# Optimization experiments

Hardware: AMD Instinct MI355X
Metric: run time of the kernel (lower is better)

## Reference

```python
import jax, jax.numpy as jnp
import numpy as np

T, N, E = 8, 5000, 160000
IN_DIM, HID, H = 64, 128, 8
D = HID // H  # head dim = 16
NC = 2
EPS = 1e-5


def layer_norm(x, g, b):
    mu = jnp.mean(x, axis=-1, keepdims=True)
    var = jnp.mean((x - mu) ** 2, axis=-1, keepdims=True)
    return (x - mu) / jnp.sqrt(var + EPS) * g + b


def setup_inputs() -> dict:
    key = jax.random.key(0)
    ks = jax.random.split(key, 24)
    p = {}
    p["x"] = jax.random.normal(ks[0], (T, N, IN_DIM), dtype=jnp.float32)
    p["edge_index"] = jax.random.randint(ks[1], (T, 2, E), 0, N, dtype=jnp.int32)
    p["noise"] = jax.random.normal(ks[2], (N, HID), dtype=jnp.float32)
    def w(k, shape, fan_in):
        return jax.random.normal(k, shape, dtype=jnp.float32) * (1.0 / np.sqrt(fan_in))
    p["W_proj"] = w(ks[3], (IN_DIM, HID), IN_DIM)
    p["b_proj"] = jnp.zeros((HID,), jnp.float32)
    p["W_gat"] = w(ks[4], (HID, HID), HID)
    p["a_src"] = w(ks[5], (H, D), D)
    p["a_dst"] = w(ks[6], (H, D), D)
    p["b_gat"] = jnp.zeros((HID,), jnp.float32)
    p["g1"] = jnp.ones((HID,), jnp.float32)
    p["be1"] = jnp.zeros((HID,), jnp.float32)
    p["W_qkv"] = w(ks[7], (3 * HID, HID), HID)
    p["b_qkv"] = jnp.zeros((3 * HID,), jnp.float32)
    p["W_o"] = w(ks[8], (HID, HID), HID)
    p["b_o"] = jnp.zeros((HID,), jnp.float32)
    p["g2"] = jnp.ones((HID,), jnp.float32)
    p["be2"] = jnp.zeros((HID,), jnp.float32)
    p["Wc1"] = w(ks[9], (HID, HID), HID)
    p["bc1"] = jnp.zeros((HID,), jnp.float32)
    p["gc"] = jnp.ones((HID,), jnp.float32)
    p["bec"] = jnp.zeros((HID,), jnp.float32)
    p["Wc2"] = w(ks[10], (HID, NC), HID)
    p["bc2"] = jnp.array([0.0, 0.1], jnp.float32)
    return p


def reference(x, edge_index, noise, W_proj, b_proj, W_gat, a_src, a_dst, b_gat,
              g1, be1, W_qkv, b_qkv, W_o, b_o, g2, be2,
              Wc1, bc1, gc, bec, Wc2, bc2):
    # per-timestep projection + ReLU: [T, N, HID]
    h = jax.nn.relu(x @ W_proj + b_proj)

    loop = jnp.arange(N, dtype=edge_index.dtype)

    def gat(h_t, ei):  # h_t: [N, HID], ei: [2, E]
        src = jnp.concatenate([ei[0], loop])  # add self loops
        dst = jnp.concatenate([ei[1], loop])
        xh = (h_t @ W_gat).reshape(N, H, D)          # [N, H, D]
        a_s = jnp.sum(xh * a_src, axis=-1)           # [N, H]
        a_d = jnp.sum(xh * a_dst, axis=-1)           # [N, H]
        e = jax.nn.leaky_relu(a_s[src] + a_d[dst], 0.2)  # [E', H]
        m = jax.ops.segment_max(e, dst, num_segments=N)
        ex = jnp.exp(e - m[dst])
        s = jax.ops.segment_sum(ex, dst, num_segments=N)
        alpha = ex / (s[dst] + 1e-16)                # segment softmax per dst/head
        out = jax.ops.segment_sum(xh[src] * alpha[..., None], dst, num_segments=N)
        return out.reshape(N, HID) + b_gat

    feats = jax.vmap(gat)(h, edge_index)             # [T, N, HID]
    nf = jnp.transpose(feats, (1, 0, 2))             # [N, T, HID] (node = batch)

    nrm = layer_norm(nf, g1, be1)
    qkv = nrm @ W_qkv.T + b_qkv                      # [N, T, 3*HID]
    q, k, v = jnp.split(qkv, 3, axis=-1)
    def heads(t):
        return t.reshape(N, T, H, D).transpose(0, 2, 1, 3)  # [N, H, T, D]
    q, k, v = heads(q), heads(k), heads(v)
    scores = jnp.einsum('nhqd,nhkd->nhqk', q, k) / jnp.sqrt(jnp.float32(D))
    attn = jax.nn.softmax(scores, axis=-1)
    ta = jnp.einsum('nhqk,nhkd->nhqd', attn, v)
    ta = ta.transpose(0, 2, 1, 3).reshape(N, T, HID) @ W_o.T + b_o

    fused = layer_norm(nf + ta, g2, be2)
    emb = fused[:, -1, :]                            # [N, HID]

    node_ids = jnp.arange(N, dtype=jnp.float32) / N
    div = jnp.sin(node_ids * 6.28) * 0.1             # [N]
    emb = emb + div[:, None] + noise * 0.05          # eval noise scale

    h1 = emb @ Wc1 + bc1
    h1 = jax.nn.gelu(layer_norm(h1, gc, bec), approximate=False)
    logits = h1 @ Wc2 + bc2                          # [N, 2]
    sinu = jnp.sin(jnp.arange(N, dtype=jnp.float32) * 0.5) * 0.2
    logits = logits.at[:, 1].add(sinu)
    return emb, logits
```

## Files before the change

kernel.cpp:

```cpp
#include <hip/hip_runtime.h>
#include <math.h>

#define T 8
#define N 5000
#define E 160000
#define EN (E + N)
#define IN_DIM 64
#define HID 128
#define H 8
#define D 16
#define NC 2
#define MT 32

__device__ __forceinline__ float leaky(float e) { return (e >= 0.0f) ? e : 0.2f * e; }

__global__ __launch_bounds__(256) void k_pg(const float* __restrict__ x,
                                            const float* __restrict__ Wp,
                                            const float* __restrict__ bp,
                                            const float* __restrict__ Wg,
                                            const float* __restrict__ asrc,
                                            const float* __restrict__ adst,
                                            float* __restrict__ xh,
                                            float* __restrict__ a_s,
                                            float* __restrict__ a_d,
                                            int* __restrict__ cursor) {
    __shared__ float xt[MT][IN_DIM];
    __shared__ float ht[MT][HID + 1];
    int row0 = blockIdx.x * MT;
    int tid = threadIdx.x;

    {
        int gi = blockIdx.x * 256 + tid;
        if (gi < T * N) cursor[gi] = 0;
    }

    for (int idx = tid; idx < MT * IN_DIM; idx += 256) {
        int r = idx >> 6, k = idx & 63;
        xt[r][k] = x[(size_t)(row0 + r) * IN_DIM + k];
    }
    __syncthreads();

    int cg = tid & 31;
    int rg = tid >> 5;
    int c0 = cg * 4, r0 = rg * 4;

    {
        float4 b4 = *(const float4*)(bp + c0);
        float a00=b4.x,a01=b4.y,a02=b4.z,a03=b4.w;
        float a10=b4.x,a11=b4.y,a12=b4.z,a13=b4.w;
        float a20=b4.x,a21=b4.y,a22=b4.z,a23=b4.w;
        float a30=b4.x,a31=b4.y,a32=b4.z,a33=b4.w;
        for (int k = 0; k < IN_DIM; ++k) {
            float4 w = *(const float4*)(Wp + (size_t)k * HID + c0);
            float x0 = xt[r0 + 0][k], x1 = xt[r0 + 1][k];
            float x2 = xt[r0 + 2][k], x3 = xt[r0 + 3][k];
            a00 += x0*w.x; a01 += x0*w.y; a02 += x0*w.z; a03 += x0*w.w;
            a10 += x1*w.x; a11 += x1*w.y; a12 += x1*w.z; a13 += x1*w.w;
            a20 += x2*w.x; a21 += x2*w.y; a22 += x2*w.z; a23 += x2*w.w;
            a30 += x3*w.x; a31 += x3*w.y; a32 += x3*w.z; a33 += x3*w.w;
        }
        ht[r0+0][c0+0]=fmaxf(a00,0.f); ht[r0+0][c0+1]=fmaxf(a01,0.f);
        ht[r0+0][c0+2]=fmaxf(a02,0.f); ht[r0+0][c0+3]=fmaxf(a03,0.f);
        ht[r0+1][c0+0]=fmaxf(a10,0.f); ht[r0+1][c0+1]=fmaxf(a11,0.f);
        ht[r0+1][c0+2]=fmaxf(a12,0.f); ht[r0+1][c0+3]=fmaxf(a13,0.f);
        ht[r0+2][c0+0]=fmaxf(a20,0.f); ht[r0+2][c0+1]=fmaxf(a21,0.f);
        ht[r0+2][c0+2]=fmaxf(a22,0.f); ht[r0+2][c0+3]=fmaxf(a23,0.f);
        ht[r0+3][c0+0]=fmaxf(a30,0.f); ht[r0+3][c0+1]=fmaxf(a31,0.f);
        ht[r0+3][c0+2]=fmaxf(a32,0.f); ht[r0+3][c0+3]=fmaxf(a33,0.f);
    }
    __syncthreads();

    float a00=0,a01=0,a02=0,a03=0, a10=0,a11=0,a12=0,a13=0;
    float a20=0,a21=0,a22=0,a23=0, a30=0,a31=0,a32=0,a33=0;
    for (int k = 0; k < HID; ++k) {
        float4 w = *(const float4*)(Wg + (size_t)k * HID + c0);
        float h0 = ht[r0 + 0][k], h1 = ht[r0 + 1][k];
        float h2 = ht[r0 + 2][k], h3 = ht[r0 + 3][k];
        a00 += h0*w.x; a01 += h0*w.y; a02 += h0*w.z; a03 += h0*w.w;
        a10 += h1*w.x; a11 += h1*w.y; a12 += h1*w.z; a13 += h1*w.w;
        a20 += h2*w.x; a21 += h2*w.y; a22 += h2*w.z; a23 += h2*w.w;
        a30 += h3*w.x; a31 += h3*w.y; a32 += h3*w.z; a33 += h3*w.w;
    }
    {
        float4 v;
        v.x=a00; v.y=a01; v.z=a02; v.w=a03;
        *(float4*)(xh + (size_t)(row0 + r0 + 0) * HID + c0) = v;
        v.x=a10; v.y=a11; v.z=a12; v.w=a13;
        *(float4*)(xh + (size_t)(row0 + r0 + 1) * HID + c0) = v;
        v.x=a20; v.y=a21; v.z=a22; v.w=a23;
        *(float4*)(xh + (size_t)(row0 + r0 + 2) * HID + c0) = v;
        v.x=a30; v.y=a31; v.z=a32; v.w=a33;
        *(float4*)(xh + (size_t)(row0 + r0 + 3) * HID + c0) = v;
    }
    __syncthreads();
    ht[r0+0][c0+0]=a00; ht[r0+0][c0+1]=a01; ht[r0+0][c0+2]=a02; ht[r0+0][c0+3]=a03;
    ht[r0+1][c0+0]=a10; ht[r0+1][c0+1]=a11; ht[r0+1][c0+2]=a12; ht[r0+1][c0+3]=a13;
    ht[r0+2][c0+0]=a20; ht[r0+2][c0+1]=a21; ht[r0+2][c0+2]=a22; ht[r0+2][c0+3]=a23;
    ht[r0+3][c0+0]=a30; ht[r0+3][c0+1]=a31; ht[r0+3][c0+2]=a32; ht[r0+3][c0+3]=a33;
    __syncthreads();

    {
        int r = tid >> 3, hh = tid & 7;
        float s1 = 0.0f, s2 = 0.0f;
        #pragma unroll
        for (int d = 0; d < D; ++d) {
            float v = ht[r][hh * D + d];
            s1 += v * asrc[hh * D + d];
            s2 += v * adst[hh * D + d];
        }
        a_s[(size_t)(row0 + r) * H + hh] = s1;
        a_d[(size_t)(row0 + r) * H + hh] = s2;
    }
}

__global__ void k_tr(const float* __restrict__ W_qkv, const float* __restrict__ W_o,
                     float* __restrict__ WTq, float* __restrict__ WoT) {
    int idx = blockIdx.x * 256 + threadIdx.x;
    if (idx < 384 * 128) {
        int j = idx >> 7, c = idx & 127;
        WTq[c * 384 + j] = W_qkv[idx];
    } else if (idx < 384 * 128 + 128 * 128) {
        int r = idx - 384 * 128;
        int j = r >> 7, k = r & 127;
        WoT[k * 128 + j] = W_o[r];
    }
}

__global__ __launch_bounds__(256) void k_hist(const int* __restrict__ ei,
                                              int* __restrict__ cursor) {
    __shared__ int hist[N];
    int t = blockIdx.x >> 3;
    int chunk = blockIdx.x & 7;
    int tid = threadIdx.x;

    for (int i = tid; i < N; i += 256) hist[i] = 0;
    __syncthreads();

    const int CS = (EN + 7) / 8;
    int i0 = chunk * CS;
    int i1 = (i0 + CS < EN) ? i0 + CS : EN;
    const int* drow = ei + (size_t)(2 * t + 1) * E;
    for (int i = i0 + tid; i < i1; i += 256) {
        int d = (i < E) ? drow[i] : (i - E);
        atomicAdd(&hist[d], 1);
    }
    __syncthreads();

    int* cur = cursor + t * N;
    for (int i = tid; i < N; i += 256) {
        int c = hist[i];
        if (c) atomicAdd(&cur[i], c);
    }
}

__global__ void k_scan(int* __restrict__ cursor, int* __restrict__ offs) {
    __shared__ int part[256];
    int t = blockIdx.x;
    int tid = threadIdx.x;
    const int CH = 20;
    int begin = tid * CH;
    int sum = 0;
    for (int k = 0; k < CH; ++k) {
        int i = begin + k;
        if (i < N) sum += cursor[t * N + i];
    }
    part[tid] = sum;
    __syncthreads();
    if (tid == 0) {
        int run = 0;
        for (int i = 0; i < 256; ++i) { int v = part[i]; part[i] = run; run += v; }
        offs[t * (N + 1) + N] = run;
    }
    __syncthreads();
    int run = part[tid];
    for (int k = 0; k < CH; ++k) {
        int i = begin + k;
        if (i < N) {
            int cnt = cursor[t * N + i];
            offs[t * (N + 1) + i] = run;
            cursor[t * N + i] = run;
            run += cnt;
        }
    }
}

__global__ __launch_bounds__(256) void k_scatter(const int* __restrict__ ei,
                                                 int* __restrict__ cursor,
                                                 int* __restrict__ csr_src) {
    const int PT = EN / 4;
    int idx = blockIdx.x * 256 + threadIdx.x;
    int t = idx / PT;
    if (t >= T) return;
    int e0 = idx - t * PT;

    const int* srow = ei + (size_t)(2 * t) * E;
    const int* drow = srow + E;
    int s[4], d[4];
    #pragma unroll
    for (int j = 0; j < 4; ++j) {
        int i = e0 + j * PT;
        if (i < E) { s[j] = srow[i]; d[j] = drow[i]; }
        else       { s[j] = d[j] = i - E; }
    }
    int* cur = cursor + t * N;
    int p[4];
    #pragma unroll
    for (int j = 0; j < 4; ++j) p[j] = atomicAdd(&cur[d[j]], 1);
    int* csb = csr_src + (size_t)t * EN;
    #pragma unroll
    for (int j = 0; j < 4; ++j) csb[p[j]] = s[j];
}

__global__ __launch_bounds__(128) void k_aggc(
        const int* __restrict__ offs, const int* __restrict__ csr_src,
        const float* __restrict__ a_s, const float* __restrict__ a_d,
        const float* __restrict__ xh, const float* __restrict__ b_gat,
        const float* __restrict__ g1, const float* __restrict__ be1,
        float* __restrict__ nrm, float* __restrict__ xlast_g) {
    int b = blockIdx.x;
    int t = b & 7;
    int dst = b >> 3;
    int tid = threadIdx.x;

    int o0 = offs[t * (N + 1) + dst];
    int o1 = offs[t * (N + 1) + dst + 1];
    int deg = o1 - o0;
    const int* esrc = csr_src + (size_t)t * EN + o0;
    const float* as_b = a_s + (size_t)t * N * H;
    const float* ad_b = a_d + (size_t)t * N * H;
    const float* xh_b = xh + (size_t)t * N * HID;

    __shared__ float lal[16][H];
    __shared__ int   lsrc[16];
    __shared__ float ws_s[2][H];
    __shared__ float pacc[2][HID];
    __shared__ float red[128];

    int eh_e = tid >> 3, eh_h = tid & 7;
    int el = tid >> 5, cg = tid & 31;
    int hg = cg >> 2;
    float adh_e = ad_b[dst * H + eh_h];

    float4 acc = {0.0f, 0.0f, 0.0f, 0.0f};
    float wpart = 0.0f;

    int ntile = (deg + 15) >> 4;
    for (int tt = 0; tt < ntile; ++tt) {
        int ej = (tt << 4) + eh_e;
        float w = 0.0f;
        int src = 0;
        if (ej < deg) {
            src = esrc[ej];
            w = expf(leaky(as_b[src * H + eh_h] + adh_e));
        }
        if (eh_h == 0) lsrc[eh_e] = src;
        lal[eh_e][eh_h] = w;
        wpart += w;
        __syncthreads();
        #pragma unroll
        for (int jj = 0; jj < 4; ++jj) {
            int j = (jj << 2) + el;
            int s = lsrc[j];
            float l = lal[j][hg];
            float4 v = *(const float4*)(xh_b + (size_t)s * HID + (cg << 2));
            acc.x += l * v.x; acc.y += l * v.y;
            acc.z += l * v.z; acc.w += l * v.w;
        }
        __syncthreads();
    }

    {
        float w = wpart;
        w += __shfl_xor(w, 8);
        w += __shfl_xor(w, 16);
        w += __shfl_xor(w, 32);
        if ((tid & 63) < 8) ws_s[tid >> 6][eh_h] = w;
    }
    acc.x += __shfl_xor(acc.x, 32);
    acc.y += __shfl_xor(acc.y, 32);
    acc.z += __shfl_xor(acc.z, 32);
    acc.w += __shfl_xor(acc.w, 32);
    if (!(tid & 32)) *(float4*)&pacc[tid >> 6][(tid & 31) << 2] = acc;
    __syncthreads();

    int hh = tid >> 4;
    float wsum = ws_s[0][hh] + ws_s[1][hh];
    float val = (pacc[0][tid] + pacc[1][tid]) / (wsum + 1e-16f);

    float v = val + b_gat[tid];
    red[tid] = v;
    __syncthreads();
    if (tid < 64) {
        float s = red[tid] + red[tid + 64];
        #pragma unroll
        for (int m = 1; m < 64; m <<= 1) s += __shfl_xor(s, m);
        if (tid == 0) red[0] = s;
    }
    __syncthreads();
    float mu = red[0] * (1.0f / HID);
    __syncthreads();
    float dv = v - mu;
    red[tid] = dv * dv;
    __syncthreads();
    if (tid < 64) {
        float s = red[tid] + red[tid + 64];
        #pragma unroll
        for (int m = 1; m < 64; m <<= 1) s += __shfl_xor(s, m);
        if (tid == 0) red[0] = s;
    }
    __syncthreads();
    float rstd = rsqrtf(red[0] * (1.0f / HID) + 1e-5f);

    nrm[(size_t)(t * N + dst) * HID + tid] = dv * rstd * g1[tid] + be1[tid];
    if (t == T - 1) xlast_g[(size_t)dst * HID + tid] = v;
}

__global__ __launch_bounds__(256) void k_qkv(const float* __restrict__ nrm,
                                             const float* __restrict__ WTq,
                                             const float* __restrict__ b_qkv,
                                             float* __restrict__ kv,
                                             float* __restrict__ qlast) {
    __shared__ float at[MT][HID];
    const int NKV = (T * N) / MT;
    int b = blockIdx.x;
    int tid = threadIdx.x;
    bool qp = (b >= NKV);
    int row0 = qp ? (b - NKV) * MT : b * MT;
    const float* src = qp ? nrm + (size_t)(T - 1) * N * HID : nrm;
    int rmax = qp ? N : T * N;

    for (int idx = tid; idx < MT * HID; idx += 256) {
        int r = idx >> 7, c = idx & 127;
        int row = row0 + r;
        at[r][c] = (row < rmax) ? src[(size_t)row * HID + c] : 0.0f;
    }
    __syncthreads();

    int cg = tid & 31, rg = tid >> 5;
    int c0 = cg * 4, r0 = rg * 4;

    int gb = qp ? 0 : 1, ge = qp ? 1 : 3;
    for (int g = gb; g < ge; ++g) {
        int co = g * 128 + c0;
        float4 b4 = *(const float4*)(b_qkv + co);
        float a00=b4.x,a01=b4.y,a02=b4.z,a03=b4.w;
        float a10=b4.x,a11=b4.y,a12=b4.z,a13=b4.w;
        float a20=b4.x,a21=b4.y,a22=b4.z,a23=b4.w;
        float a30=b4.x,a31=b4.y,a32=b4.z,a33=b4.w;
        for (int k = 0; k < HID; ++k) {
            float4 w = *(const float4*)(WTq + (size_t)k * 384 + co);
            float e0 = at[r0 + 0][k], e1 = at[r0 + 1][k];
            float e2 = at[r0 + 2][k], e3 = at[r0 + 3][k];
            a00 += e0*w.x; a01 += e0*w.y; a02 += e0*w.z; a03 += e0*w.w;
            a10 += e1*w.x; a11 += e1*w.y; a12 += e1*w.z; a13 += e1*w.w;
            a20 += e2*w.x; a21 += e2*w.y; a22 += e2*w.z; a23 += e2*w.w;
            a30 += e3*w.x; a31 += e3*w.y; a32 += e3*w.z; a33 += e3*w.w;
        }
        float4 v0; v0.x=a00; v0.y=a01; v0.z=a02; v0.w=a03;
        float4 v1; v1.x=a10; v1.y=a11; v1.z=a12; v1.w=a13;
        float4 v2; v2.x=a20; v2.y=a21; v2.z=a22; v2.w=a23;
        float4 v3; v3.x=a30; v3.y=a31; v3.z=a32; v3.w=a33;
        if (qp) {
            if (row0 + r0 + 0 < N) *(float4*)(qlast + (size_t)(row0+r0+0) * HID + c0) = v0;
            if (row0 + r0 + 1 < N) *(float4*)(qlast + (size_t)(row0+r0+1) * HID + c0) = v1;
            if (row0 + r0 + 2 < N) *(float4*)(qlast + (size_t)(row0+r0+2) * HID + c0) = v2;
            if (row0 + r0 + 3 < N) *(float4*)(qlast + (size_t)(row0+r0+3) * HID + c0) = v3;
        } else {
            int coff = (g - 1) * 128 + c0;
            *(float4*)(kv + (size_t)(row0+r0+0) * 256 + coff) = v0;
            *(float4*)(kv + (size_t)(row0+r0+1) * 256 + coff) = v1;
            *(float4*)(kv + (size_t)(row0+r0+2) * 256 + coff) = v2;
            *(float4*)(kv + (size_t)(row0+r0+3) * 256 + coff) = v3;
        }
    }
}

__global__ __launch_bounds__(128) void k_node(
        const float* __restrict__ kv, const float* __restrict__ qlast,
        const float* __restrict__ xlast_g,
        const float* __restrict__ WoT, const float* __restrict__ b_o,
        const float* __restrict__ g2, const float* __restrict__ be2,
        const float* __restrict__ noise, float* __restrict__ out) {
    __shared__ float ql[HID];
    __shared__ float kl[H][T][D];
    __shared__ float vl[H][T][D];
    __shared__ float attn_l[H][T];
    __shared__ float ta[HID];
    __shared__ float red[128];

    int n = blockIdx.x;
    int tid = threadIdx.x;
    int hh = tid >> 4, dd = tid & 15;

    ql[tid] = qlast[(size_t)n * HID + tid];
    #pragma unroll
    for (int tt = 0; tt < T; ++tt) {
        const float* kvr = kv + (size_t)(tt * N + n) * 256;
        kl[hh][tt][dd] = kvr[tid];
        vl[hh][tt][dd] = kvr[128 + tid];
    }
    float xl = xlast_g[(size_t)n * HID + tid];
    __syncthreads();

    if (tid < H) {
        int hq = tid;
        float sc[T];
        float mx = -1e30f;
        #pragma unroll
        for (int tk = 0; tk < T; ++tk) {
            float a = 0.0f;
            #pragma unroll
            for (int d2 = 0; d2 < D; ++d2) a += ql[hq * D + d2] * kl[hq][tk][d2];
            a *= 0.25f;
            sc[tk] = a;
            mx = fmaxf(mx, a);
        }
        float ssum = 0.0f;
        #pragma unroll
        for (int tk = 0; tk < T; ++tk) { sc[tk] = expf(sc[tk] - mx); ssum += sc[tk]; }
        float inv = 1.0f / ssum;
        #pragma unroll
        for (int tk = 0; tk < T; ++tk) attn_l[hq][tk] = sc[tk] * inv;
    }
    __syncthreads();

    {
        float a = 0.0f;
        #pragma unroll
        for (int tk = 0; tk < T; ++tk) a += attn_l[hh][tk] * vl[hh][tk][dd];
        ta[tid] = a;
    }
    __syncthreads();

    float o = b_o[tid];
    #pragma unroll 8
    for (int k = 0; k < HID; k += 4) {
        float4 t4 = *(const float4*)&ta[k];
        o += t4.x * WoT[(size_t)(k + 0) * 128 + tid]
           + t4.y * WoT[(size_t)(k + 1) * 128 + tid]
           + t4.z * WoT[(size_t)(k + 2) * 128 + tid]
           + t4.w * WoT[(size_t)(k + 3) * 128 + tid];
    }
    float x2 = xl + o;

    red[tid] = x2;
    __syncthreads();
    if (tid < 64) {
        float s = red[tid] + red[tid + 64];
        #pragma unroll
        for (int m = 1; m < 64; m <<= 1) s += __shfl_xor(s, m);
        if (tid == 0) red[0] = s;
    }
    __syncthreads();
    float mu2 = red[0] * (1.0f / HID);
    __syncthreads();
    float d2v = x2 - mu2;
    red[tid] = d2v * d2v;
    __syncthreads();
    if (tid < 64) {
        float s = red[tid] + red[tid + 64];
        #pragma unroll
        for (int m = 1; m < 64; m <<= 1) s += __shfl_xor(s, m);
        if (tid == 0) red[0] = s;
    }
    __syncthreads();
    float rstd2 = rsqrtf(red[0] * (1.0f / HID) + 1e-5f);

    float div = sinf(((float)n / (float)N) * 6.28f) * 0.1f;
    float emb = d2v * rstd2 * g2[tid] + be2[tid]
              + div + noise[(size_t)n * HID + tid] * 0.05f;
    out[(size_t)n * HID + tid] = emb;
}

__global__ __launch_bounds__(256) void k_cls(const float* __restrict__ emb,
                                             const float* __restrict__ Wc1,
                                             const float* __restrict__ bc1,
                                             const float* __restrict__ gc,
                                             const float* __restrict__ bec,
                                             const float* __restrict__ Wc2,
                                             const float* __restrict__ bc2,
                                             float* __restrict__ out) {
    __shared__ float et[MT][HID];
    __shared__ float h1t[MT][HID + 1];
    int row0 = blockIdx.x * MT;
    int tid = threadIdx.x;

    for (int idx = tid; idx < MT * HID; idx += 256) {
        int r = idx >> 7, c = idx & 127;
        int row = row0 + r;
        et[r][c] = (row < N) ? emb[(size_t)row * HID + c] : 0.0f;
    }
    __syncthreads();

    {
        int cg = tid & 31, rg = tid >> 5;
        int c0 = cg * 4, r0 = rg * 4;
        float4 b4 = *(const float4*)(bc1 + c0);
        float a00=b4.x,a01=b4.y,a02=b4.z,a03=b4.w;
        float a10=b4.x,a11=b4.y,a12=b4.z,a13=b4.w;
        float a20=b4.x,a21=b4.y,a22=b4.z,a23=b4.w;
        float a30=b4.x,a31=b4.y,a32=b4.z,a33=b4.w;
        for (int k = 0; k < HID; ++k) {
            float4 w = *(const float4*)(Wc1 + (size_t)k * HID + c0);
            float e0 = et[r0 + 0][k], e1 = et[r0 + 1][k];
            float e2 = et[r0 + 2][k], e3 = et[r0 + 3][k];
            a00 += e0*w.x; a01 += e0*w.y; a02 += e0*w.z; a03 += e0*w.w;
            a10 += e1*w.x; a11 += e1*w.y; a12 += e1*w.z; a13 += e1*w.w;
            a20 += e2*w.x; a21 += e2*w.y; a22 += e2*w.z; a23 += e2*w.w;
            a30 += e3*w.x; a31 += e3*w.y; a32 += e3*w.z; a33 += e3*w.w;
        }
        h1t[r0+0][c0+0]=a00; h1t[r0+0][c0+1]=a01; h1t[r0+0][c0+2]=a02; h1t[r0+0][c0+3]=a03;
        h1t[r0+1][c0+0]=a10; h1t[r0+1][c0+1]=a11; h1t[r0+1][c0+2]=a12; h1t[r0+1][c0+3]=a13;
        h1t[r0+2][c0+0]=a20; h1t[r0+2][c0+1]=a21; h1t[r0+2][c0+2]=a22; h1t[r0+2][c0+3]=a23;
        h1t[r0+3][c0+0]=a30; h1t[r0+3][c0+1]=a31; h1t[r0+3][c0+2]=a32; h1t[r0+3][c0+3]=a33;
    }
    __syncthreads();

    {
        int r = tid >> 3, l = tid & 7;
        float p = 0.0f;
        #pragma unroll
        for (int k = 0; k < 16; ++k) p += h1t[r][l + 8 * k];
        #pragma unroll
        for (int m = 1; m < 8; m <<= 1) p += __shfl_xor(p, m);
        float mu = p * (1.0f / HID);
        float v = 0.0f;
        #pragma unroll
        for (int k = 0; k < 16; ++k) { float d = h1t[r][l + 8 * k] - mu; v += d * d; }
        #pragma unroll
        for (int m = 1; m < 8; m <<= 1) v += __shfl_xor(v, m);
        float rstd = rsqrtf(v * (1.0f / HID) + 1e-5f);
        #pragma unroll
        for (int k = 0; k < 16; ++k) {
            int c = l + 8 * k;
            float lnv = (h1t[r][c] - mu) * rstd * gc[c] + bec[c];
            h1t[r][c] = 0.5f * lnv * (1.0f + erff(lnv * 0.70710678118f));
        }
    }
    __syncthreads();

    if (tid < MT * NC) {
        int r = tid >> 1, j = tid & 1;
        int row = row0 + r;
        if (row < N) {
            float acc = bc2[j];
            #pragma unroll 8
            for (int c = 0; c < HID; ++c) acc += h1t[r][c] * Wc2[c * NC + j];
            if (j == 1) acc += sinf((float)row * 0.5f) * 0.2f;
            out[(size_t)N * HID + (size_t)row * NC + j] = acc;
        }
    }
}

extern "C" void kernel_launch(void* const* d_in, const int* in_sizes, int n_in,
                              void* d_out, int out_size, void* d_ws, size_t ws_size,
                              hipStream_t stream) {
    const float* x      = (const float*)d_in[0];
    const int*   ei     = (const int*)d_in[1];
    const float* noise  = (const float*)d_in[2];
    const float* W_proj = (const float*)d_in[3];
    const float* b_proj = (const float*)d_in[4];
    const float* W_gat  = (const float*)d_in[5];
    const float* a_src  = (const float*)d_in[6];
    const float* a_dst  = (const float*)d_in[7];
    const float* b_gat  = (const float*)d_in[8];
    const float* g1     = (const float*)d_in[9];
    const float* be1    = (const float*)d_in[10];
    const float* W_qkv  = (const float*)d_in[11];
    const float* b_qkv  = (const float*)d_in[12];
    const float* W_o    = (const float*)d_in[13];
    const float* b_o    = (const float*)d_in[14];
    const float* g2     = (const float*)d_in[15];
    const float* be2    = (const float*)d_in[16];
    const float* Wc1    = (const float*)d_in[17];
    const float* bc1    = (const float*)d_in[18];
    const float* gc     = (const float*)d_in[19];
    const float* bec    = (const float*)d_in[20];
    const float* Wc2    = (const float*)d_in[21];
    const float* bc2    = (const float*)d_in[22];
    float* out = (float*)d_out;

    float* xh     = (float*)d_ws;
    float* nrm    = xh + 5120000;
    float* a_s    = nrm + 5120000;
    float* a_d    = a_s + 320000;
    int*   offs    = (int*)(a_d + 320000);
    int*   cursor  = offs + 40008;
    int*   csr_src = cursor + 40000;
    float* WTq    = (float*)(csr_src + 1320000);
    float* WoT    = WTq + 49152;
    float* kv     = WoT + 16384;
    float* qlast  = kv + 10240000;
    float* xlastg = qlast + 640000;

    k_tr<<<(384 * 128 + 128 * 128 + 255) / 256, 256, 0, stream>>>(W_qkv, W_o, WTq, WoT);

    k_pg<<<T * N / MT, 256, 0, stream>>>(x, W_proj, b_proj, W_gat, a_src, a_dst,
                                         xh, a_s, a_d, cursor);

    k_hist<<<T * 8, 256, 0, stream>>>(ei, cursor);
    k_scan<<<T, 256, 0, stream>>>(cursor, offs);
    k_scatter<<<(T * (EN / 4) + 255) / 256, 256, 0, stream>>>(ei, cursor, csr_src);

    k_aggc<<<T * N, 128, 0, stream>>>(offs, csr_src, a_s, a_d, xh,
                                      b_gat, g1, be1, nrm, xlastg);

    k_qkv<<<(T * N) / MT + (N + MT - 1) / MT, 256, 0, stream>>>(nrm, WTq, b_qkv,
                                                                kv, qlast);

    k_node<<<N, 128, 0, stream>>>(kv, qlast, xlastg, WoT, b_o,
                                  g2, be2, noise, out);

    k_cls<<<(N + MT - 1) / MT, 256, 0, stream>>>(out, Wc1, bc1, gc, bec, Wc2, bc2, out);
}
```

Measured before the change: 393.4 us.

## Fuse QKV projection and temporal attention into one per-node-group kernel

Changes the nrm layout to node-major [N,T,HID] so each block can load all timesteps for 4 nodes, then computes K/V for those rows and Q for the last step in shared memory. Attention, output projection, residual and LayerNorm follow in the same kernel. This removes the large global kv/qlast intermediate buffers and one kernel launch. In exchange, k_aggc now writes with a strided pattern, and the LayerNorm switches to a single-pass E[x^2]-mu^2 variance.

```diff
diff --git a/kernel.cpp b/kernel.cpp
--- a/kernel.cpp
+++ b/kernel.cpp
@@ -11,6 +11,7 @@
 #define D 16
 #define NC 2
 #define MT 32
+#define NB 4
 
 __device__ __forceinline__ float leaky(float e) { return (e >= 0.0f) ? e : 0.2f * e; }
 
@@ -311,37 +312,43 @@
     __syncthreads();
     float rstd = rsqrtf(red[0] * (1.0f / HID) + 1e-5f);
 
-    nrm[(size_t)(t * N + dst) * HID + tid] = dv * rstd * g1[tid] + be1[tid];
+    nrm[(size_t)(dst * T + t) * HID + tid] = dv * rstd * g1[tid] + be1[tid];
     if (t == T - 1) xlast_g[(size_t)dst * HID + tid] = v;
 }
 
-__global__ __launch_bounds__(256) void k_qkv(const float* __restrict__ nrm,
-                                             const float* __restrict__ WTq,
-                                             const float* __restrict__ b_qkv,
-                                             float* __restrict__ kv,
-                                             float* __restrict__ qlast) {
-    __shared__ float at[MT][HID];
-    const int NKV = (T * N) / MT;
-    int b = blockIdx.x;
+__global__ __launch_bounds__(256) void k_fuse(
+        const float* __restrict__ nrm,
+        const float* __restrict__ WTq,
+        const float* __restrict__ b_qkv,
+        const float* __restrict__ xlast_g,
+        const float* __restrict__ WoT,
+        const float* __restrict__ b_o,
+        const float* __restrict__ g2, const float* __restrict__ be2,
+        const float* __restrict__ noise, float* __restrict__ out) {
+    __shared__ float at[NB * T][HID];
+    __shared__ float kvl[2][NB * T][HID + 2];
+    __shared__ float ql[NB][HID];
+    float* attn_s = &at[0][0];
+    float* ta_s   = &at[0][0] + 256;
+
+    int n0 = blockIdx.x * NB;
     int tid = threadIdx.x;
-    bool qp = (b >= NKV);
-    int row0 = qp ? (b - NKV) * MT : b * MT;
-    const float* src = qp ? nrm + (size_t)(T - 1) * N * HID : nrm;
-    int rmax = qp ? N : T * N;
-
-    for (int idx = tid; idx < MT * HID; idx += 256) {
-        int r = idx >> 7, c = idx & 127;
-        int row = row0 + r;
-        at[r][c] = (row < rmax) ? src[(size_t)row * HID + c] : 0.0f;
+
+    {
+        const float* src = nrm + (size_t)n0 * T * HID;
+        for (int idx = tid; idx < NB * T * 32; idx += 256) {
+            int r = idx >> 5, c4 = (idx & 31) << 2;
+            *(float4*)&at[r][c4] = *(const float4*)(src + (size_t)r * HID + c4);
+        }
     }
     __syncthreads();
 
     int cg = tid & 31, rg = tid >> 5;
     int c0 = cg * 4, r0 = rg * 4;
 
-    int gb = qp ? 0 : 1, ge = qp ? 1 : 3;
-    for (int g = gb; g < ge; ++g) {
-        int co = g * 128 + c0;
+    #pragma unroll
+    for (int g = 0; g < 2; ++g) {
+        int co = 128 + g * 128 + c0;
         float4 b4 = *(const float4*)(b_qkv + co);
         float a00=b4.x,a01=b4.y,a02=b4.z,a03=b4.w;
         float a10=b4.x,a11=b4.y,a12=b4.z,a13=b4.w;
@@ -349,127 +356,106 @@
         float a30=b4.x,a31=b4.y,a32=b4.z,a33=b4.w;
         for (int k = 0; k < HID; ++k) {
             float4 w = *(const float4*)(WTq + (size_t)k * 384 + co);
-            float e0 = at[r0 + 0][k], e1 = at[r0 + 1][k];
-            float e2 = at[r0 + 2][k], e3 = at[r0 + 3][k];
+            float e0 = at[r0+0][k], e1 = at[r0+1][k];
+            float e2 = at[r0+2][k], e3 = at[r0+3][k];
             a00 += e0*w.x; a01 += e0*w.y; a02 += e0*w.z; a03 += e0*w.w;
             a10 += e1*w.x; a11 += e1*w.y; a12 += e1*w.z; a13 += e1*w.w;
             a20 += e2*w.x; a21 += e2*w.y; a22 += e2*w.z; a23 += e2*w.w;
             a30 += e3*w.x; a31 += e3*w.y; a32 += e3*w.z; a33 += e3*w.w;
         }
-        float4 v0; v0.x=a00; v0.y=a01; v0.z=a02; v0.w=a03;
-        float4 v1; v1.x=a10; v1.y=a11; v1.z=a12; v1.w=a13;
-        float4 v2; v2.x=a20; v2.y=a21; v2.z=a22; v2.w=a23;
-        float4 v3; v3.x=a30; v3.y=a31; v3.z=a32; v3.w=a33;
-        if (qp) {
-            if (row0 + r0 + 0 < N) *(float4*)(qlast + (size_t)(row0+r0+0) * HID + c0) = v0;
-            if (row0 + r0 + 1 < N) *(float4*)(qlast + (size_t)(row0+r0+1) * HID + c0) = v1;
-            if (row0 + r0 + 2 < N) *(float4*)(qlast + (size_t)(row0+r0+2) * HID + c0) = v2;
-            if (row0 + r0 + 3 < N) *(float4*)(qlast + (size_t)(row0+r0+3) * HID + c0) = v3;
-        } else {
-            int coff = (g - 1) * 128 + c0;
-            *(float4*)(kv + (size_t)(row0+r0+0) * 256 + coff) = v0;
-            *(float4*)(kv + (size_t)(row0+r0+1) * 256 + coff) = v1;
-            *(float4*)(kv + (size_t)(row0+r0+2) * 256 + coff) = v2;
-            *(float4*)(kv + (size_t)(row0+r0+3) * 256 + coff) = v3;
-        }
-    }
-}
-
-__global__ __launch_bounds__(128) void k_node(
-        const float* __restrict__ kv, const float* __restrict__ qlast,
-        const float* __restrict__ xlast_g,
-        const float* __restrict__ WoT, const float* __restrict__ b_o,
-        const float* __restrict__ g2, const float* __restrict__ be2,
-        const float* __restrict__ noise, float* __restrict__ out) {
-    __shared__ float ql[HID];
-    __shared__ float kl[H][T][D];
-    __shared__ float vl[H][T][D];
-    __shared__ float attn_l[H][T];
-    __shared__ float ta[HID];
-    __shared__ float red[128];
-
-    int n = blockIdx.x;
-    int tid = threadIdx.x;
-    int hh = tid >> 4, dd = tid & 15;
-
-    ql[tid] = qlast[(size_t)n * HID + tid];
-    #pragma unroll
-    for (int tt = 0; tt < T; ++tt) {
-        const float* kvr = kv + (size_t)(tt * N + n) * 256;
-        kl[hh][tt][dd] = kvr[tid];
-        vl[hh][tt][dd] = kvr[128 + tid];
-    }
-    float xl = xlast_g[(size_t)n * HID + tid];
-    __syncthreads();
-
-    if (tid < H) {
-        int hq = tid;
-        float sc[T];
-        float mx = -1e30f;
+        kvl[g][r0+0][c0+0]=a00; kvl[g][r0+0][c0+1]=a01; kvl[g][r0+0][c0+2]=a02; kvl[g][r0+0][c0+3]=a03;
+        kvl[g][r0+1][c0+0]=a10; kvl[g][r0+1][c0+1]=a11; kvl[g][r0+1][c0+2]=a12; kvl[g][r0+1][c0+3]=a13;
+        kvl[g][r0+2][c0+0]=a20; kvl[g][r0+2][c0+1]=a21; kvl[g][r0+2][c0+2]=a22; kvl[g][r0+2][c0+3]=a23;
+        kvl[g][r0+3][c0+0]=a30; kvl[g][r0+3][c0+1]=a31; kvl[g][r0+3][c0+2]=a32; kvl[g][r0+3][c0+3]=a33;
+    }
+
+    {
+        int u = tid >> 6, c = tid & 63;
+        float q0 = b_qkv[c], q1 = b_qkv[c + 64];
+        const float* ar = at[u * T + (T - 1)];
+        for (int k = 0; k < HID; ++k) {
+            float av = ar[k];
+            q0 += av * WTq[(size_t)k * 384 + c];
+            q1 += av * WTq[(size_t)k * 384 + c + 64];
+        }
+        ql[u][c] = q0;
+        ql[u][c + 64] = q1;
+    }
+    __syncthreads();
+
+    {
+        int u = tid >> 6, h = (tid >> 3) & 7, tk = tid & 7;
+        float qf[D];
+        #pragma unroll
+        for (int d = 0; d < D; ++d) qf[d] = ql[u][h * D + d];
+        const float* kr = &kvl[0][u * T + tk][h * D];
+        float a = 0.0f;
+        #pragma unroll
+        for (int d = 0; d < D; ++d) a += qf[d] * kr[d];
+        a *= 0.25f;
+        float mx = a;
+        mx = fmaxf(mx, __shfl_xor(mx, 1));
+        mx = fmaxf(mx, __shfl_xor(mx, 2));
+        mx = fmaxf(mx, __shfl_xor(mx, 4));
+        float w = expf(a - mx);
+        float ssum = w;
+        ssum += __shfl_xor(ssum, 1);
+        ssum += __shfl_xor(ssum, 2);
+        ssum += __shfl_xor(ssum, 4);
+        attn_s[u * 64 + h * 8 + tk] = w / ssum;
+    }
+    __syncthreads();
+
+    {
+        int u = tid >> 6, c = tid & 63;
+        int ha = c >> 4, hb = (c + 64) >> 4;
+        const float* aa = attn_s + u * 64 + ha * 8;
+        const float* ab = attn_s + u * 64 + hb * 8;
+        float sa = 0.0f, sb = 0.0f;
         #pragma unroll
         for (int tk = 0; tk < T; ++tk) {
-            float a = 0.0f;
-            #pragma unroll
-            for (int d2 = 0; d2 < D; ++d2) a += ql[hq * D + d2] * kl[hq][tk][d2];
-            a *= 0.25f;
-            sc[tk] = a;
-            mx = fmaxf(mx, a);
-        }
-        float ssum = 0.0f;
-        #pragma unroll
-        for (int tk = 0; tk < T; ++tk) { sc[tk] = expf(sc[tk] - mx); ssum += sc[tk]; }
-        float inv = 1.0f / ssum;
-        #pragma unroll
-        for (int tk = 0; tk < T; ++tk) attn_l[hq][tk] = sc[tk] * inv;
-    }
-    __syncthreads();
-
-    {
-        float a = 0.0f;
-        #pragma unroll
-        for (int tk = 0; tk < T; ++tk) a += attn_l[hh][tk] * vl[hh][tk][dd];
-        ta[tid] = a;
-    }
-    __syncthreads();
-
-    float o = b_o[tid];
-    #pragma unroll 8
-    for (int k = 0; k < HID; k += 4) {
-        float4 t4 = *(const float4*)&ta[k];
-        o += t4.x * WoT[(size_t)(k + 0) * 128 + tid]
-           + t4.y * WoT[(size_t)(k + 1) * 128 + tid]
-           + t4.z * WoT[(size_t)(k + 2) * 128 + tid]
-           + t4.w * WoT[(size_t)(k + 3) * 128 + tid];
-    }
-    float x2 = xl + o;
-
-    red[tid] = x2;
-    __syncthreads();
-    if (tid < 64) {
-        float s = red[tid] + red[tid + 64];
-        #pragma unroll
-        for (int m = 1; m < 64; m <<= 1) s += __shfl_xor(s, m);
-        if (tid == 0) red[0] = s;
-    }
-    __syncthreads();
-    float mu2 = red[0] * (1.0f / HID);
-    __syncthreads();
-    float d2v = x2 - mu2;
-    red[tid] = d2v * d2v;
-    __syncthreads();
-    if (tid < 64) {
-        float s = red[tid] + red[tid + 64];
-        #pragma unroll
-        for (int m = 1; m < 64; m <<= 1) s += __shfl_xor(s, m);
-        if (tid == 0) red[0] = s;
-    }
-    __syncthreads();
-    float rstd2 = rsqrtf(red[0] * (1.0f / HID) + 1e-5f);
-
-    float div = sinf(((float)n / (float)N) * 6.28f) * 0.1f;
-    float emb = d2v * rstd2 * g2[tid] + be2[tid]
-              + div + noise[(size_t)n * HID + tid] * 0.05f;
-    out[(size_t)n * HID + tid] = emb;
+            const float* vr = kvl[1][u * T + tk];
+            sa += aa[tk] * vr[c];
+            sb += ab[tk] * vr[c + 64];
+        }
+        ta_s[u * 128 + c] = sa;
+        ta_s[u * 128 + c + 64] = sb;
+    }
+    __syncthreads();
+
+    {
+        int u = tid >> 6, c = tid & 63;
+        int n = n0 + u;
+        float o0 = b_o[c], o1 = b_o[c + 64];
+        const float* tar = ta_s + u * 128;
+        #pragma unroll 8
+        for (int k = 0; k < HID; k += 4) {
+            float t0 = tar[k], t1 = tar[k+1], t2 = tar[k+2], t3 = tar[k+3];
+            o0 += t0 * WoT[(size_t)(k+0)*128 + c]  + t1 * WoT[(size_t)(k+1)*128 + c]
+                + t2 * WoT[(size_t)(k+2)*128 + c]  + t3 * WoT[(size_t)(k+3)*128 + c];
+            o1 += t0 * WoT[(size_t)(k+0)*128 + c+64] + t1 * WoT[(size_t)(k+1)*128 + c+64]
+                + t2 * WoT[(size_t)(k+2)*128 + c+64] + t3 * WoT[(size_t)(k+3)*128 + c+64];
+        }
+        float xa = xlast_g[(size_t)n * HID + c];
+        float xb = xlast_g[(size_t)n * HID + c + 64];
+        float x2a = xa + o0, x2b = xb + o1;
+        float s = x2a + x2b, qs = x2a * x2a + x2b * x2b;
+        #pragma unroll
+        for (int m = 1; m < 64; m <<= 1) {
+            s  += __shfl_xor(s, m);
+            qs += __shfl_xor(qs, m);
+        }
+        float mu = s * (1.0f / HID);
+        float var = qs * (1.0f / HID) - mu * mu;
+        float rstd = rsqrtf(var + 1e-5f);
+        float dv = sinf(((float)n / (float)N) * 6.28f) * 0.1f;
+        out[(size_t)n * HID + c] =
+            (x2a - mu) * rstd * g2[c] + be2[c] + dv
+            + noise[(size_t)n * HID + c] * 0.05f;
+        out[(size_t)n * HID + c + 64] =
+            (x2b - mu) * rstd * g2[c + 64] + be2[c + 64] + dv
+            + noise[(size_t)n * HID + c + 64] * 0.05f;
+    }
 }
 
 __global__ __launch_bounds__(256) void k_cls(const float* __restrict__ emb,
@@ -589,9 +575,7 @@
     int*   csr_src = cursor + 40000;
     float* WTq    = (float*)(csr_src + 1320000);
     float* WoT    = WTq + 49152;
-    float* kv     = WoT + 16384;
-    float* qlast  = kv + 10240000;
-    float* xlastg = qlast + 640000;
+    float* xlastg = WoT + 16384;
 
     k_tr<<<(384 * 128 + 128 * 128 + 255) / 256, 256, 0, stream>>>(W_qkv, W_o, WTq, WoT);
 
@@ -605,11 +589,8 @@
     k_aggc<<<T * N, 128, 0, stream>>>(offs, csr_src, a_s, a_d, xh,
                                       b_gat, g1, be1, nrm, xlastg);
 
-    k_qkv<<<(T * N) / MT + (N + MT - 1) / MT, 256, 0, stream>>>(nrm, WTq, b_qkv,
-                                                                kv, qlast);
-
-    k_node<<<N, 128, 0, stream>>>(kv, qlast, xlastg, WoT, b_o,
-                                  g2, be2, noise, out);
+    k_fuse<<<N / NB, 256, 0, stream>>>(nrm, WTq, b_qkv, xlastg, WoT, b_o,
+                                       g2, be2, noise, out);
 
     k_cls<<<(N + MT - 1) / MT, 256, 0, stream>>>(out, Wc1, bc1, gc, bec, Wc2, bc2, out);
 }
```

Result: faster. 383.5 us (-2.5%).
